# Kernel tuning notes

Measured on AMD Instinct MI355X. Metric: run time of the kernel, lower is better.

The kernel has to match this reference:

```python
import jax, jax.numpy as jnp
import numpy as np

B_SZ, L, D_MODEL = 2, 2048, 1024
EXPAND, D_STATE, D_CONV = 2, 16, 4
D_INNER = D_MODEL * EXPAND
DT_RANK = -(-D_MODEL // 16)  # ceil(d_model/16) = 64


def setup_inputs() -> dict:
    key = jax.random.key(0)
    ks = jax.random.split(key, 8)
    s = 0.02
    return {
        "u": jax.random.normal(ks[0], (B_SZ, L, D_MODEL), jnp.float32),
        "W_in": jax.random.normal(ks[1], (2 * D_INNER, D_MODEL), jnp.float32) * s,
        "W_out": jax.random.normal(ks[2], (D_MODEL, D_INNER), jnp.float32) * s,
        "conv_w": jax.random.normal(ks[3], (D_INNER, D_CONV), jnp.float32) * s,  # depthwise kernel (weight.squeeze(1))
        "conv_b": jax.random.normal(ks[4], (D_INNER,), jnp.float32) * s,
        "W_x": jax.random.normal(ks[5], (DT_RANK + 2 * D_STATE, D_INNER), jnp.float32) * s,
        "W_dt": jax.random.normal(ks[6], (D_INNER, DT_RANK), jnp.float32) * s,
        "b_dt": jax.random.normal(ks[7], (D_INNER,), jnp.float32) * s,
        "A_log": jnp.tile(jnp.log(jnp.arange(1, D_STATE + 1, dtype=jnp.float32)), (D_INNER, 1)),
        "D_param": jnp.ones((D_INNER,), jnp.float32),
    }


def _causal_conv(x, w, b):
    # x: [B, L, Di], w: [Di, K] depthwise, b: [Di]. Left-pad K-1 => causal.
    K = w.shape[1]
    Lx = x.shape[1]
    xp = jnp.pad(x, ((0, 0), (K - 1, 0), (0, 0)))
    acc = b
    for k in range(K):  # K=4, tiny fixed unroll
        acc = acc + xp[:, k:k + Lx, :] * w[:, k]
    return acc


def reference(u, W_in, W_out, conv_w, conv_b, W_x, W_dt, b_dt, A_log, D_param):
    d_inner = D_param.shape[0]
    N = A_log.shape[1]
    dt_rank = W_dt.shape[1]

    xz = u @ W_in.T                       # [B, L, 2*Di]
    x_in, z = xz[..., :d_inner], xz[..., d_inner:]
    x = jax.nn.silu(_causal_conv(x_in, conv_w, conv_b))  # [B, L, Di]

    x_p = x @ W_x.T                       # [B, L, dt_rank + 2N]
    dt_r = x_p[..., :dt_rank]
    Bm = x_p[..., dt_rank:dt_rank + N]    # [B, L, N]
    Cm = x_p[..., dt_rank + N:]           # [B, L, N]
    dt = jax.nn.softplus(dt_r @ W_dt.T + b_dt)  # [B, L, Di]

    A = -jnp.exp(A_log)                   # [Di, N]

    def step(h, inp):
        dt_t, B_t, C_t, x_t = inp         # [B,Di], [B,N], [B,N], [B,Di]
        dA = jnp.exp(dt_t[:, :, None] * A)             # [B, Di, N]
        h = dA * h + (dt_t * x_t)[:, :, None] * B_t[:, None, :]
        y_t = jnp.einsum('bdn,bn->bd', h, C_t)
        return h, y_t

    h0 = jnp.zeros((u.shape[0], d_inner, N), u.dtype)
    seq = (dt.transpose(1, 0, 2), Bm.transpose(1, 0, 2),
           Cm.transpose(1, 0, 2), x.transpose(1, 0, 2))
    _, ys = jax.lax.scan(step, h0, seq)   # ys: [L, B, Di]

    y = ys.transpose(1, 0, 2) + D_param * x
    y = y * jax.nn.silu(z)
    return y @ W_out.T                    # [B, L, d_model]
```

## Files before the change

kernel.cpp:

```cpp
#include <hip/hip_runtime.h>
#include <hip/hip_bf16.h>
#include <cstdint>
#include <cstddef>


typedef __bf16 bf16x8 __attribute__((ext_vector_type(8)));
typedef __bf16 bf16x4 __attribute__((ext_vector_type(4)));
typedef float f32x4 __attribute__((ext_vector_type(4)));
typedef unsigned int u32x4 __attribute__((ext_vector_type(4)));

#define LOG2E 1.44269504088896f

__device__ __forceinline__ bf16x8 cvt8(const float* __restrict__ p) {
    f32x4 a = *(const f32x4*)p;
    f32x4 b = *(const f32x4*)(p + 4);
    bf16x8 o;
    o[0] = (__bf16)a[0]; o[1] = (__bf16)a[1]; o[2] = (__bf16)a[2]; o[3] = (__bf16)a[3];
    o[4] = (__bf16)b[0]; o[5] = (__bf16)b[1]; o[6] = (__bf16)b[2]; o[7] = (__bf16)b[3];
    return o;
}

__device__ __forceinline__ void gll16(const __bf16* g, __bf16* l) {
    __builtin_amdgcn_global_load_lds(
        (const __attribute__((address_space(1))) void*)g,
        (__attribute__((address_space(3))) void*)l, 16, 0, 0);
}

__device__ __forceinline__ uint32_t packbf(__bf16 lo, __bf16 hi) {
    uint16_t a = __builtin_bit_cast(uint16_t, lo);
    uint16_t b = __builtin_bit_cast(uint16_t, hi);
    return (uint32_t)a | ((uint32_t)b << 16);
}
__device__ __forceinline__ float lo2f(uint32_t u) { return __builtin_bit_cast(float, u << 16); }
__device__ __forceinline__ float hi2f(uint32_t u) { return __builtin_bit_cast(float, u & 0xffff0000u); }

template<int CTRL>
__device__ __forceinline__ float qp_add(float v) {
    int r = __builtin_amdgcn_update_dpp(0, __builtin_bit_cast(int, v), CTRL, 0xF, 0xF, true);
    return v + __builtin_bit_cast(float, r);
}

__global__ void cvt_all_kernel(const float* __restrict__ u,   __bf16* __restrict__ ub,
                               const float* __restrict__ wi,  __bf16* __restrict__ wib,
                               const float* __restrict__ wo,  __bf16* __restrict__ wob,
                               const float* __restrict__ wx,  __bf16* __restrict__ wxb,
                               const float* __restrict__ wdt, __bf16* __restrict__ wdtb,
                               const float* __restrict__ cw,  float* __restrict__ cwT) {
    int i = blockIdx.x * 256 + threadIdx.x;
    if (i < 1351680) {
        const float* s; __bf16* d; int off;
        if (i < 524288)                { s = u;   d = ub;   off = i; }
        else if (i < 1048576)          { s = wi;  d = wib;  off = i - 524288; }
        else if (i < 1310720)          { s = wo;  d = wob;  off = i - 1048576; }
        else if (i < 1335296)          { s = wx;  d = wxb;  off = i - 1310720; }
        else                           { s = wdt; d = wdtb; off = i - 1335296; }
        *(bf16x8*)(d + (size_t)off * 8) = cvt8(s + (size_t)off * 8);
    } else {
        int off = (i - 1351680) * 8;
#pragma unroll
        for (int e = 0; e < 8; ++e) {
            int s = off + e;
            cwT[(s & 3) * 2048 + (s >> 2)] = cw[s];
        }
    }
}

__global__ __launch_bounds__(256, 3) void gemm_async_bf(const __bf16* __restrict__ A,
                                                        const __bf16* __restrict__ Bw,
                                                        __bf16* __restrict__ C,
                                                        int K, int ldc) {
    __shared__ __bf16 As[128][32];
    __shared__ __bf16 Bs[128][32];
    const int tid = threadIdx.x, lane = tid & 63, wave = tid >> 6;
    const int m0 = blockIdx.x * 128, n0 = blockIdx.y * 128;
    const int wm = (wave >> 1) * 64, wn = (wave & 1) * 64;
    const int mrow = lane & 15, kq = (lane >> 4) * 8;
    const int sr = wave * 32 + (lane >> 2);
    const int sk = (lane & 3) * 8;
    const __bf16* Ag0 = A + (size_t)(m0 + sr) * K + sk;
    const __bf16* Ag1 = Ag0 + (size_t)16 * K;
    const __bf16* Bg0 = Bw + (size_t)(n0 + sr) * K + sk;
    const __bf16* Bg1 = Bg0 + (size_t)16 * K;
    __bf16* La0 = &As[wave * 32][0];
    __bf16* La1 = &As[wave * 32 + 16][0];
    __bf16* Lb0 = &Bs[wave * 32][0];
    __bf16* Lb1 = &Bs[wave * 32 + 16][0];
    f32x4 acc[4][4] = {};
    for (int k0 = 0; k0 < K; k0 += 32) {
        gll16(Ag0 + k0, La0);
        gll16(Ag1 + k0, La1);
        gll16(Bg0 + k0, Lb0);
        gll16(Bg1 + k0, Lb1);
        __syncthreads();
        bf16x8 af[4], bfr[4];
#pragma unroll
        for (int i = 0; i < 4; ++i) af[i]  = *(const bf16x8*)&As[wm + i * 16 + mrow][kq];
#pragma unroll
        for (int j = 0; j < 4; ++j) bfr[j] = *(const bf16x8*)&Bs[wn + j * 16 + mrow][kq];
#pragma unroll
        for (int i = 0; i < 4; ++i)
#pragma unroll
            for (int j = 0; j < 4; ++j)
                acc[i][j] = __builtin_amdgcn_mfma_f32_16x16x32_bf16(af[i], bfr[j], acc[i][j], 0, 0, 0);
        __syncthreads();
    }
    const int col = lane & 15;
    const int rb = (lane >> 4) * 4;
#pragma unroll
    for (int i = 0; i < 4; ++i)
#pragma unroll
        for (int j = 0; j < 4; ++j)
#pragma unroll
            for (int r = 0; r < 4; ++r)
                C[(size_t)(m0 + wm + i * 16 + rb + r) * ldc + n0 + wn + j * 16 + col] =
                    (__bf16)acc[i][j][r];
}

__global__ __launch_bounds__(256, 3) void gemm_splitk(const __bf16* __restrict__ A,
                                                      const __bf16* __restrict__ Bw,
                                                      float* __restrict__ P) {
    __shared__ __bf16 As[128][32];
    __shared__ __bf16 Bs[128][32];
    const int tid = threadIdx.x, lane = tid & 63, wave = tid >> 6;
    const int m0 = blockIdx.x * 128, n0 = blockIdx.y * 128;
    const int kz = blockIdx.z * 1024;
    const int wm = (wave >> 1) * 64, wn = (wave & 1) * 64;
    const int mrow = lane & 15, kq = (lane >> 4) * 8;
    const int sr = wave * 32 + (lane >> 2);
    const int sk = (lane & 3) * 8;
    const __bf16* Ag0 = A + (size_t)(m0 + sr) * 2048 + kz + sk;
    const __bf16* Ag1 = Ag0 + (size_t)16 * 2048;
    const __bf16* Bg0 = Bw + (size_t)(n0 + sr) * 2048 + kz + sk;
    const __bf16* Bg1 = Bg0 + (size_t)16 * 2048;
    __bf16* La0 = &As[wave * 32][0];
    __bf16* La1 = &As[wave * 32 + 16][0];
    __bf16* Lb0 = &Bs[wave * 32][0];
    __bf16* Lb1 = &Bs[wave * 32 + 16][0];
    f32x4 acc[4][4] = {};
    for (int k0 = 0; k0 < 1024; k0 += 32) {
        gll16(Ag0 + k0, La0);
        gll16(Ag1 + k0, La1);
        gll16(Bg0 + k0, Lb0);
        gll16(Bg1 + k0, Lb1);
        __syncthreads();
        bf16x8 af[4], bfr[4];
#pragma unroll
        for (int i = 0; i < 4; ++i) af[i]  = *(const bf16x8*)&As[wm + i * 16 + mrow][kq];
#pragma unroll
        for (int j = 0; j < 4; ++j) bfr[j] = *(const bf16x8*)&Bs[wn + j * 16 + mrow][kq];
#pragma unroll
        for (int i = 0; i < 4; ++i)
#pragma unroll
            for (int j = 0; j < 4; ++j)
                acc[i][j] = __builtin_amdgcn_mfma_f32_16x16x32_bf16(af[i], bfr[j], acc[i][j], 0, 0, 0);
        __syncthreads();
    }
    const int col = lane & 15;
    const int rb = (lane >> 4) * 4;
    float* Pz = P + (size_t)blockIdx.z * 4096 * 1024;
#pragma unroll
    for (int i = 0; i < 4; ++i)
#pragma unroll
        for (int j = 0; j < 4; ++j)
#pragma unroll
            for (int r = 0; r < 4; ++r)
                Pz[(size_t)(m0 + wm + i * 16 + rb + r) * 1024 + n0 + wn + j * 16 + col] =
                    acc[i][j][r];
}

__global__ void add2_kernel(const float* __restrict__ P, float* __restrict__ out) {
    int i = blockIdx.x * 256 + threadIdx.x;
    f32x4 a = *(const f32x4*)(P + (size_t)i * 4);
    f32x4 b = *(const f32x4*)(P + (size_t)4096 * 1024 + (size_t)i * 4);
    *(f32x4*)(out + (size_t)i * 4) = a + b;
}

__global__ void conv_silu_kernel(const __bf16* __restrict__ xz,
                                 const float* __restrict__ cwT,
                                 const float* __restrict__ cb,
                                 __bf16* __restrict__ x) {
    int tid = threadIdx.x;
    int r = blockIdx.x;
    int l = r & 2047;
    int d = tid * 8;

    float acc[8];
    {
        f32x4 b0 = *(const f32x4*)(cb + d);
        f32x4 b1 = *(const f32x4*)(cb + d + 4);
#pragma unroll
        for (int i = 0; i < 4; ++i) { acc[i] = b0[i]; acc[4 + i] = b1[i]; }
    }

#pragma unroll
    for (int dlt = 0; dlt < 4; ++dlt) {
        if (l - dlt >= 0) {
            bf16x8 v = *(const bf16x8*)(xz + (size_t)(r - dlt) * 4096 + d);
            f32x4 w0 = *(const f32x4*)(cwT + (3 - dlt) * 2048 + d);
            f32x4 w1 = *(const f32x4*)(cwT + (3 - dlt) * 2048 + d + 4);
#pragma unroll
            for (int i = 0; i < 4; ++i) {
                acc[i]     = fmaf((float)v[i],     w0[i], acc[i]);
                acc[4 + i] = fmaf((float)v[4 + i], w1[i], acc[4 + i]);
            }
        }
    }
    bf16x8 o;
#pragma unroll
    for (int i = 0; i < 8; ++i) {
        float s = acc[i];
        s = s / (1.f + __expf(-s));
        o[i] = (__bf16)s;
    }
    *(bf16x8*)(x + (size_t)r * 2048 + d) = o;
}

__global__ __launch_bounds__(256, 2) void gemm_xp_split(const __bf16* __restrict__ A,
                                                        const __bf16* __restrict__ Bw,
                                                        float* __restrict__ P) {
    __shared__ __bf16 As[64][64];
    __shared__ __bf16 Bs[96][64];
    const int tid = threadIdx.x;
    const int lane = tid & 63;
    const int wave = tid >> 6;
    const int m0 = blockIdx.x * 64;
    const int kb = blockIdx.y * 256;
    const int mrow = lane & 15;
    const int kq = (lane >> 4) * 8;

    f32x4 acc[6] = {};

    for (int k0 = kb; k0 < kb + 256; k0 += 64) {
#pragma unroll
        for (int r = 0; r < 2; ++r) {
            int e = r * 256 + tid;
            int row = e >> 3, kc = e & 7;
            *(bf16x8*)&As[row][kc * 8] =
                *(const bf16x8*)(A + (size_t)(m0 + row) * 2048 + k0 + kc * 8);
        }
#pragma unroll
        for (int r = 0; r < 3; ++r) {
            int e = r * 256 + tid;
            int row = e >> 3, kc = e & 7;
            *(bf16x8*)&Bs[row][kc * 8] =
                *(const bf16x8*)(Bw + (size_t)row * 2048 + k0 + kc * 8);
        }
        __syncthreads();
#pragma unroll
        for (int kc = 0; kc < 2; ++kc) {
            bf16x8 af = *(const bf16x8*)&As[wave * 16 + mrow][kc * 32 + kq];
#pragma unroll
            for (int j = 0; j < 6; ++j) {
                bf16x8 bfr = *(const bf16x8*)&Bs[j * 16 + mrow][kc * 32 + kq];
                acc[j] = __builtin_amdgcn_mfma_f32_16x16x32_bf16(af, bfr, acc[j], 0, 0, 0);
            }
        }
        __syncthreads();
    }
    const int col = lane & 15;
    const int rb = (lane >> 4) * 4;
    float* Pb = P + (size_t)blockIdx.y * 4096 * 96;
#pragma unroll
    for (int j = 0; j < 6; ++j)
#pragma unroll
        for (int r = 0; r < 4; ++r)
            Pb[(size_t)(m0 + wave * 16 + rb + r) * 96 + j * 16 + col] = acc[j][r];
}

__global__ void xp_reduce(const float* __restrict__ P, __bf16* __restrict__ xp) {
    int m = blockIdx.x, c = threadIdx.x;
    if (c < 96) {
        float s = 0.f;
#pragma unroll
        for (int k = 0; k < 8; ++k) s += P[(size_t)k * 4096 * 96 + (size_t)m * 96 + c];
        xp[(size_t)m * 96 + c] = (__bf16)s;
    }
}

__global__ __launch_bounds__(256, 2) void gemm_dt(const __bf16* __restrict__ xp,
                                                  const __bf16* __restrict__ Wdt,
                                                  const float* __restrict__ bdt,
                                                  __bf16* __restrict__ dt) {
    const int tid = threadIdx.x;
    const int lane = tid & 63;
    const int wave = tid >> 6;
    const int m0 = blockIdx.x * 128 + (wave >> 1) * 64;
    const int n0 = blockIdx.y * 128 + (wave & 1) * 64;
    const int mrow = lane & 15;
    const int kq = (lane >> 4) * 8;

    f32x4 acc[4][4] = {};
#pragma unroll
    for (int kc = 0; kc < 2; ++kc) {
        bf16x8 af[4], bfr[4];
#pragma unroll
        for (int i = 0; i < 4; ++i)
            af[i] = *(const bf16x8*)(xp + (size_t)(m0 + i * 16 + mrow) * 96 + kc * 32 + kq);
#pragma unroll
        for (int j = 0; j < 4; ++j)
            bfr[j] = *(const bf16x8*)(Wdt + (size_t)(n0 + j * 16 + mrow) * 64 + kc * 32 + kq);
#pragma unroll
        for (int i = 0; i < 4; ++i)
#pragma unroll
            for (int j = 0; j < 4; ++j)
                acc[i][j] = __builtin_amdgcn_mfma_f32_16x16x32_bf16(af[i], bfr[j], acc[i][j], 0, 0, 0);
    }
    const int col = lane & 15;
    const int rb = (lane >> 4) * 4;
#pragma unroll
    for (int i = 0; i < 4; ++i)
#pragma unroll
        for (int j = 0; j < 4; ++j) {
            int cc = n0 + j * 16 + col;
            float bias = bdt[cc];
#pragma unroll
            for (int r = 0; r < 4; ++r) {
                float v = acc[i][j][r] + bias;
                float sp = (v > 20.f) ? v : log1pf(__expf(v));
                dt[(size_t)(m0 + i * 16 + rb + r) * 4096 + cc] = (__bf16)sp;
            }
        }
}

__global__ __launch_bounds__(256, 6) void scan_p1(const __bf16* __restrict__ xz,
                                                  const __bf16* __restrict__ xq,
                                                  const __bf16* __restrict__ xp,
                                                  const float* __restrict__ A_log,
                                                  float* __restrict__ h_end,
                                                  float* __restrict__ dtsum) {
    __shared__ uint32_t s_dtx[64][64];
    __shared__ __bf16 s_B[64][16];
    const int tid = threadIdx.x;
    const int bi = blockIdx.x;
    const int b = bi >> 10, c = (bi >> 5) & 31, d0 = (bi & 31) * 64;
    const int row0 = b * 2048 + c * 64;

    const int lane = tid & 63, wave = tid >> 6;
    const int dcol = wave * 16 + (lane >> 2);
    const int d = d0 + dcol;
    const int ng = lane & 3;
    f32x4 Al = *(const f32x4*)(A_log + (size_t)d * 16 + ng * 4);
    float Adn2[4];
#pragma unroll
    for (int j = 0; j < 4; ++j) Adn2[j] = -__expf(Al[j]) * LOG2E;

    {
        int t = tid >> 2, g = (tid & 3) * 4;
        *(bf16x4*)&s_B[t][g] = *(const bf16x4*)(xp + (size_t)(row0 + t) * 96 + 64 + g);
    }
#pragma unroll
    for (int i = 0; i < 4; ++i) {
        int w = i * 256 + tid;
        int t = w >> 4, g = (w & 15) * 4;
        size_t r = (size_t)(row0 + t);
        bf16x4 dt4 = *(const bf16x4*)(xz + r * 4096 + d0 + g);
        bf16x4 x4  = *(const bf16x4*)(xq + r * 2048 + d0 + g);
        u32x4 o;
#pragma unroll
        for (int k = 0; k < 4; ++k) o[k] = packbf(dt4[k], x4[k]);
        *(u32x4*)&s_dtx[t][g] = o;
    }
    __syncthreads();

    float h[4] = {0.f, 0.f, 0.f, 0.f};
    float ds = 0.f;
#pragma unroll 8
    for (int t = 0; t < 64; ++t) {
        uint32_t u = s_dtx[t][dcol];
        float dt = lo2f(u), x = hi2f(u);
        bf16x4 B4 = *(const bf16x4*)&s_B[t][ng * 4];
        float p = dt * x;
#pragma unroll
        for (int j = 0; j < 4; ++j) {
            float dA = exp2f(dt * Adn2[j]);
            h[j] = fmaf(dA, h[j], p * (float)B4[j]);
        }
        ds += dt;
    }
    size_t base = (size_t)(b * 32 + c) * 2048 + d;
    f32x4 hv = {h[0], h[1], h[2], h[3]};
    *(f32x4*)(h_end + base * 16 + ng * 4) = hv;
    if (ng == 0) dtsum[base] = ds;
}

__global__ __launch_bounds__(256) void scan_p2(const float* __restrict__ A_log,
                                               const float* __restrict__ dtsum,
                                               const float* __restrict__ h_end,
                                               float* __restrict__ h_in) {
    int idx = blockIdx.x * 256 + threadIdx.x;
    int b = idx >> 15, rem = idx & 32767;
    int d = rem >> 4;
    float Adn = -__expf(A_log[rem]);
    float h = 0.f;
#pragma unroll
    for (int c = 0; c < 32; ++c) {
        size_t base = ((size_t)(b * 32 + c) << 15) + rem;
        h_in[base] = h;
        float P = __expf(Adn * dtsum[((size_t)(b * 32 + c) << 11) + d]);
        h = fmaf(P, h, h_end[base]);
    }
}

__global__ __launch_bounds__(256, 4) void scan_p3(const __bf16* __restrict__ xz,
                                                  __bf16* __restrict__ xq,
                                                  const __bf16* __restrict__ xp,
                                                  const float* __restrict__ A_log,
                                                  const float* __restrict__ Dp,
                                                  const float* __restrict__ h_in) {
    __shared__ uint32_t s_dtx[64][64];
    __shared__ uint32_t s_BC[64][16];
    __shared__ __bf16 s_y[64][64];
    const int tid = threadIdx.x;
    const int bi = blockIdx.x;
    const int b = bi >> 10, c = (bi >> 5) & 31, d0 = (bi & 31) * 64;
    const int row0 = b * 2048 + c * 64;

    const int lane = tid & 63, wave = tid >> 6;
    const int dcol = wave * 16 + (lane >> 2);
    const int d = d0 + dcol;
    const int ng = lane & 3;
    f32x4 Al = *(const f32x4*)(A_log + (size_t)d * 16 + ng * 4);
    float Adn2[4];
#pragma unroll
    for (int j = 0; j < 4; ++j) Adn2[j] = -__expf(Al[j]) * LOG2E;
    const float Dd = Dp[d];
    f32x4 h = *(const f32x4*)(h_in + ((size_t)(b * 32 + c) * 2048 + d) * 16 + ng * 4);

    {
        int t = tid >> 2, g = (tid & 3) * 4;
        bf16x4 B4 = *(const bf16x4*)(xp + (size_t)(row0 + t) * 96 + 64 + g);
        bf16x4 C4 = *(const bf16x4*)(xp + (size_t)(row0 + t) * 96 + 80 + g);
        u32x4 o;
#pragma unroll
        for (int k = 0; k < 4; ++k) o[k] = packbf(B4[k], C4[k]);
        *(u32x4*)&s_BC[t][g] = o;
    }
#pragma unroll
    for (int i = 0; i < 4; ++i) {
        int w = i * 256 + tid;
        int t = w >> 4, g = (w & 15) * 4;
        size_t r = (size_t)(row0 + t);
        bf16x4 dt4 = *(const bf16x4*)(xz + r * 4096 + d0 + g);
        bf16x4 x4  = *(const bf16x4*)(xq + r * 2048 + d0 + g);
        u32x4 o;
#pragma unroll
        for (int k = 0; k < 4; ++k) o[k] = packbf(dt4[k], x4[k]);
        *(u32x4*)&s_dtx[t][g] = o;
    }
    __syncthreads();

#pragma unroll 8
    for (int t = 0; t < 64; ++t) {
        uint32_t u = s_dtx[t][dcol];
        float dt = lo2f(u), x = hi2f(u);
        u32x4 bc = *(const u32x4*)&s_BC[t][ng * 4];
        float p = dt * x;
        float cs;
#pragma unroll
        for (int j = 0; j < 4; ++j) {
            float Bv = lo2f(bc[j]), Cv = hi2f(bc[j]);
            float dA = exp2f(dt * Adn2[j]);
            h[j] = fmaf(dA, h[j], p * Bv);
            cs = (j == 0) ? h[0] * Cv : fmaf(h[j], Cv, cs);
        }
        cs = qp_add<0xB1>(cs);
        cs = qp_add<0x4E>(cs);
        if (ng == 0) s_y[t][dcol] = (__bf16)fmaf(Dd, x, cs);
    }
    __syncthreads();
#pragma unroll
    for (int i = 0; i < 2; ++i) {
        int w = i * 256 + tid;
        int t = w >> 3, g = (w & 7) * 8;
        bf16x8 z8 = *(const bf16x8*)(xz + (size_t)(row0 + t) * 4096 + 2048 + d0 + g);
        bf16x8 y8 = *(bf16x8*)&s_y[t][g];
        bf16x8 o;
#pragma unroll
        for (int k = 0; k < 8; ++k) {
            float zv = (float)z8[k];
            float yv = (float)y8[k] * (zv / (1.f + __expf(-zv)));
            o[k] = (__bf16)yv;
        }
        *(bf16x8*)(xq + (size_t)(row0 + t) * 2048 + d0 + g) = o;
    }
}

extern "C" void kernel_launch(void* const* d_in, const int* in_sizes, int n_in,
                              void* d_out, int out_size, void* d_ws, size_t ws_size,
                              hipStream_t stream) {
    const float* u      = (const float*)d_in[0];
    const float* W_in   = (const float*)d_in[1];
    const float* W_out  = (const float*)d_in[2];
    const float* conv_w = (const float*)d_in[3];
    const float* conv_b = (const float*)d_in[4];
    const float* W_x    = (const float*)d_in[5];
    const float* W_dt   = (const float*)d_in[6];
    const float* b_dt   = (const float*)d_in[7];
    const float* A_log  = (const float*)d_in[8];
    const float* D_p    = (const float*)d_in[9];
    float* out = (float*)d_out;

    __bf16* xz   = (__bf16*)d_ws;
    __bf16* xq   = xz  + (size_t)4096 * 4096;
    __bf16* xp   = xq  + (size_t)4096 * 2048;
    __bf16* Wib  = xp  + (size_t)4096 * 96;
    __bf16* Wob  = Wib + (size_t)4096 * 1024;
    __bf16* Wxb  = Wob + (size_t)1024 * 2048;
    __bf16* Wdtb = Wxb + (size_t)96 * 2048;

    __bf16* ub    = (__bf16*)d_out;
    float* xpart  = (float*)d_out;
    float* h_end  = (float*)d_out;
    float* h_in   = (float*)d_out + 2097152;
    float* cwT    = (float*)d_out + 3407872;
    float* dtsum  = (float*)Wib;
    float* gpart  = (float*)xz;

    cvt_all_kernel<<<5284, 256, 0, stream>>>(u, ub, W_in, Wib, W_out, Wob,
                                             W_x, Wxb, W_dt, Wdtb, conv_w, cwT);

    gemm_async_bf<<<dim3(32, 32), 256, 0, stream>>>(ub, Wib, xz, 1024, 4096);
    conv_silu_kernel<<<4096, 256, 0, stream>>>(xz, cwT, conv_b, xq);
    gemm_xp_split<<<dim3(64, 8), 256, 0, stream>>>(xq, Wxb, xpart);
    xp_reduce<<<4096, 128, 0, stream>>>(xpart, xp);
    gemm_dt<<<dim3(32, 16), 256, 0, stream>>>(xp, Wdtb, b_dt, xz);
    scan_p1<<<2048, 256, 0, stream>>>(xz, xq, xp, A_log, h_end, dtsum);
    scan_p2<<<256, 256, 0, stream>>>(A_log, dtsum, h_end, h_in);
    scan_p3<<<2048, 256, 0, stream>>>(xz, xq, xp, A_log, D_p, h_in);
    gemm_splitk<<<dim3(32, 8, 2), 256, 0, stream>>>(xq, Wob, gpart);
    add2_kernel<<<4096, 256, 0, stream>>>(gpart, out);
}
```

Baseline: 333.8 us.

## Fuse three-phase chunked scan into one cooperative kernel with grid syncs

Replaces the three scan kernels with a single cooperative kernel. Each block loads its 128-step chunk of dt, x, B and C into LDS once, runs the local scan, grid-syncs, does the inter-chunk carry on the first 256 blocks, grid-syncs again, then applies the correction and the z gating in place. This avoids reloading chunk data and the extra launches, at the cost of grid-wide barriers and an occupancy requirement of 4 blocks per CU, with a fallback path when that requirement is not met. The depthwise conv kernel also now handles 4 rows per block with a sliding window, so overlapping rows are reused instead of reloaded.

```diff
diff --git a/kernel.cpp b/kernel.cpp
--- a/kernel.cpp
+++ b/kernel.cpp
@@ -1,8 +1,11 @@
 #include <hip/hip_runtime.h>
 #include <hip/hip_bf16.h>
+#include <hip/hip_cooperative_groups.h>
 #include <cstdint>
 #include <cstddef>
 
+
+namespace cg = cooperative_groups;
 
 typedef __bf16 bf16x8 __attribute__((ext_vector_type(8)));
 typedef __bf16 bf16x4 __attribute__((ext_vector_type(4)));
@@ -33,6 +36,10 @@
 }
 __device__ __forceinline__ float lo2f(uint32_t u) { return __builtin_bit_cast(float, u << 16); }
 __device__ __forceinline__ float hi2f(uint32_t u) { return __builtin_bit_cast(float, u & 0xffff0000u); }
+__device__ __forceinline__ uint32_t f2hi(float y, uint32_t u) {
+    uint16_t yb = __builtin_bit_cast(uint16_t, (__bf16)y);
+    return (u & 0xffffu) | ((uint32_t)yb << 16);
+}
 
 template<int CTRL>
 __device__ __forceinline__ float qp_add(float v) {
@@ -179,40 +186,53 @@
                                  const float* __restrict__ cwT,
                                  const float* __restrict__ cb,
                                  __bf16* __restrict__ x) {
-    int tid = threadIdx.x;
-    int r = blockIdx.x;
-    int l = r & 2047;
-    int d = tid * 8;
-
-    float acc[8];
-    {
-        f32x4 b0 = *(const f32x4*)(cb + d);
-        f32x4 b1 = *(const f32x4*)(cb + d + 4);
+    const int r0 = blockIdx.x * 4;
+    const int d = threadIdx.x * 8;
+    const bool first = (r0 & 2047) == 0;
+
+    f32x4 w0[4], w1[4];
+#pragma unroll
+    for (int k = 0; k < 4; ++k) {
+        w0[k] = *(const f32x4*)(cwT + k * 2048 + d);
+        w1[k] = *(const f32x4*)(cwT + k * 2048 + d + 4);
+    }
+    f32x4 b0 = *(const f32x4*)(cb + d);
+    f32x4 b1 = *(const f32x4*)(cb + d + 4);
+
+    bf16x8 win[4];
+#pragma unroll
+    for (int i = 0; i < 3; ++i) {
+        if (first) {
+#pragma unroll
+            for (int k = 0; k < 8; ++k) win[i][k] = (__bf16)0.f;
+        } else {
+            win[i] = *(const bf16x8*)(xz + (size_t)(r0 - 3 + i) * 4096 + d);
+        }
+    }
+#pragma unroll
+    for (int rr = 0; rr < 4; ++rr) {
+        win[(rr + 3) & 3] = *(const bf16x8*)(xz + (size_t)(r0 + rr) * 4096 + d);
+        float acc[8];
 #pragma unroll
         for (int i = 0; i < 4; ++i) { acc[i] = b0[i]; acc[4 + i] = b1[i]; }
-    }
-
-#pragma unroll
-    for (int dlt = 0; dlt < 4; ++dlt) {
-        if (l - dlt >= 0) {
-            bf16x8 v = *(const bf16x8*)(xz + (size_t)(r - dlt) * 4096 + d);
-            f32x4 w0 = *(const f32x4*)(cwT + (3 - dlt) * 2048 + d);
-            f32x4 w1 = *(const f32x4*)(cwT + (3 - dlt) * 2048 + d + 4);
+#pragma unroll
+        for (int k = 0; k < 4; ++k) {
+            bf16x8 v = win[(rr + k) & 3];
 #pragma unroll
             for (int i = 0; i < 4; ++i) {
-                acc[i]     = fmaf((float)v[i],     w0[i], acc[i]);
-                acc[4 + i] = fmaf((float)v[4 + i], w1[i], acc[4 + i]);
+                acc[i]     = fmaf((float)v[i],     w0[k][i], acc[i]);
+                acc[4 + i] = fmaf((float)v[4 + i], w1[k][i], acc[4 + i]);
             }
         }
-    }
-    bf16x8 o;
-#pragma unroll
-    for (int i = 0; i < 8; ++i) {
-        float s = acc[i];
-        s = s / (1.f + __expf(-s));
-        o[i] = (__bf16)s;
-    }
-    *(bf16x8*)(x + (size_t)r * 2048 + d) = o;
+        bf16x8 o;
+#pragma unroll
+        for (int i = 0; i < 8; ++i) {
+            float s = acc[i];
+            s = s / (1.f + __expf(-s));
+            o[i] = (__bf16)s;
+        }
+        *(bf16x8*)(x + (size_t)(r0 + rr) * 2048 + d) = o;
+    }
 }
 
 __global__ __launch_bounds__(256, 2) void gemm_xp_split(const __bf16* __restrict__ A,
@@ -320,6 +340,146 @@
                 dt[(size_t)(m0 + i * 16 + rb + r) * 4096 + cc] = (__bf16)sp;
             }
         }
+}
+
+__global__ __launch_bounds__(256, 4) void scan_fused(const __bf16* __restrict__ xz,
+                                                     __bf16* __restrict__ xq,
+                                                     const __bf16* __restrict__ xp,
+                                                     const float* __restrict__ A_log,
+                                                     const float* __restrict__ Dp,
+                                                     float* __restrict__ h_end,
+                                                     float* __restrict__ dtsum,
+                                                     float* __restrict__ h_in) {
+    __shared__ uint32_t s_dtx[128][64];
+    __shared__ uint32_t s_BC[128][16];
+    const int tid = threadIdx.x;
+    const int bi = blockIdx.x;
+    const int b = bi >> 9, c = (bi >> 5) & 15, d0 = (bi & 31) * 64;
+    const int row0 = b * 2048 + c * 128;
+
+    const int lane = tid & 63, wave = tid >> 6;
+    const int dcol = wave * 16 + (lane >> 2);
+    const int d = d0 + dcol;
+    const int ng = lane & 3;
+    f32x4 Al = *(const f32x4*)(A_log + (size_t)d * 16 + ng * 4);
+    float Adn2[4];
+#pragma unroll
+    for (int j = 0; j < 4; ++j) Adn2[j] = -__expf(Al[j]) * LOG2E;
+    const float Dd = Dp[d];
+
+#pragma unroll
+    for (int i = 0; i < 8; ++i) {
+        int w = i * 256 + tid;
+        int t = w >> 4, g = (w & 15) * 4;
+        size_t r = (size_t)(row0 + t);
+        bf16x4 dt4 = *(const bf16x4*)(xz + r * 4096 + d0 + g);
+        bf16x4 x4  = *(const bf16x4*)(xq + r * 2048 + d0 + g);
+        u32x4 o;
+#pragma unroll
+        for (int k = 0; k < 4; ++k) o[k] = packbf(dt4[k], x4[k]);
+        *(u32x4*)&s_dtx[t][g] = o;
+    }
+#pragma unroll
+    for (int i = 0; i < 2; ++i) {
+        int w = i * 256 + tid;
+        int t = w >> 2, g = (w & 3) * 4;
+        bf16x4 B4 = *(const bf16x4*)(xp + (size_t)(row0 + t) * 96 + 64 + g);
+        bf16x4 C4 = *(const bf16x4*)(xp + (size_t)(row0 + t) * 96 + 80 + g);
+        u32x4 o;
+#pragma unroll
+        for (int k = 0; k < 4; ++k) o[k] = packbf(B4[k], C4[k]);
+        *(u32x4*)&s_BC[t][g] = o;
+    }
+    __syncthreads();
+
+    {
+        float h[4] = {0.f, 0.f, 0.f, 0.f};
+        float ds = 0.f;
+#pragma unroll 4
+        for (int t = 0; t < 128; ++t) {
+            uint32_t u = s_dtx[t][dcol];
+            float dt = lo2f(u), x = hi2f(u);
+            u32x4 bc = *(const u32x4*)&s_BC[t][ng * 4];
+            float p = dt * x;
+            float cs;
+#pragma unroll
+            for (int j = 0; j < 4; ++j) {
+                float Bv = lo2f(bc[j]), Cv = hi2f(bc[j]);
+                float dA = exp2f(dt * Adn2[j]);
+                h[j] = fmaf(dA, h[j], p * Bv);
+                cs = (j == 0) ? h[0] * Cv : fmaf(h[j], Cv, cs);
+            }
+            ds += dt;
+            cs = qp_add<0xB1>(cs);
+            cs = qp_add<0x4E>(cs);
+            if (ng == 0) s_dtx[t][dcol] = f2hi(fmaf(Dd, x, cs), u);
+        }
+        size_t base = (size_t)(b * 16 + c) * 2048 + d;
+        f32x4 hv = {h[0], h[1], h[2], h[3]};
+        *(f32x4*)(h_end + base * 16 + ng * 4) = hv;
+        if (ng == 0) dtsum[base] = ds;
+    }
+
+    cg::this_grid().sync();
+
+    if (bi < 256) {
+        int idx = bi * 256 + tid;
+        int bb = idx >> 15, rem = idx & 32767;
+        int dd = rem >> 4;
+        float Adn = -__expf(A_log[rem]);
+        float h = 0.f;
+#pragma unroll
+        for (int cc = 0; cc < 16; ++cc) {
+            size_t base = ((size_t)(bb * 16 + cc) << 15) + rem;
+            h_in[base] = h;
+            float P = __expf(Adn * dtsum[((size_t)(bb * 16 + cc) << 11) + dd]);
+            h = fmaf(P, h, h_end[base]);
+        }
+    }
+
+    cg::this_grid().sync();
+
+    {
+        f32x4 hin = *(const f32x4*)(h_in + ((size_t)(b * 16 + c) * 2048 + d) * 16 + ng * 4);
+        float Sd = 0.f;
+#pragma unroll 4
+        for (int t = 0; t < 128; ++t) {
+            uint32_t u = s_dtx[t][dcol];
+            float dt = lo2f(u);
+            Sd += dt;
+            u32x4 bc = *(const u32x4*)&s_BC[t][ng * 4];
+            float corr;
+#pragma unroll
+            for (int j = 0; j < 4; ++j) {
+                float Cv = hi2f(bc[j]);
+                float e = exp2f(Sd * Adn2[j]);
+                corr = (j == 0) ? e * hin[0] * Cv : fmaf(e * hin[j], Cv, corr);
+            }
+            corr = qp_add<0xB1>(corr);
+            corr = qp_add<0x4E>(corr);
+            if (ng == 0) {
+                float yraw = hi2f(u) + corr;
+                s_dtx[t][dcol] = __builtin_bit_cast(uint32_t, yraw);
+            }
+        }
+    }
+    __syncthreads();
+
+#pragma unroll
+    for (int i = 0; i < 8; ++i) {
+        int w = i * 256 + tid;
+        int t = w >> 4, g = (w & 15) * 4;
+        u32x4 yv = *(const u32x4*)&s_dtx[t][g];
+        bf16x4 z4 = *(const bf16x4*)(xz + (size_t)(row0 + t) * 4096 + 2048 + d0 + g);
+        bf16x4 o;
+#pragma unroll
+        for (int k = 0; k < 4; ++k) {
+            float zv = (float)z4[k];
+            float yv_f = __builtin_bit_cast(float, yv[k]);
+            o[k] = (__bf16)(yv_f * (zv / (1.f + __expf(-zv))));
+        }
+        *(bf16x4*)(xq + (size_t)(row0 + t) * 2048 + d0 + g) = o;
+    }
 }
 
 __global__ __launch_bounds__(256, 6) void scan_p1(const __bf16* __restrict__ xz,
@@ -520,13 +680,30 @@
                                              W_x, Wxb, W_dt, Wdtb, conv_w, cwT);
 
     gemm_async_bf<<<dim3(32, 32), 256, 0, stream>>>(ub, Wib, xz, 1024, 4096);
-    conv_silu_kernel<<<4096, 256, 0, stream>>>(xz, cwT, conv_b, xq);
+    conv_silu_kernel<<<1024, 256, 0, stream>>>(xz, cwT, conv_b, xq);
     gemm_xp_split<<<dim3(64, 8), 256, 0, stream>>>(xq, Wxb, xpart);
     xp_reduce<<<4096, 128, 0, stream>>>(xpart, xp);
     gemm_dt<<<dim3(32, 16), 256, 0, stream>>>(xp, Wdtb, b_dt, xz);
-    scan_p1<<<2048, 256, 0, stream>>>(xz, xq, xp, A_log, h_end, dtsum);
-    scan_p2<<<256, 256, 0, stream>>>(A_log, dtsum, h_end, h_in);
-    scan_p3<<<2048, 256, 0, stream>>>(xz, xq, xp, A_log, D_p, h_in);
+
+    int maxb = 0;
+    hipError_t qerr = hipOccupancyMaxActiveBlocksPerMultiprocessor(&maxb, scan_fused, 256, 0);
+    bool coop_ok = (qerr == hipSuccess) && (maxb >= 4);
+    if (coop_ok) {
+        const __bf16* xz_c = xz; __bf16* xq_c = xq; const __bf16* xp_c = xp;
+        const float* al_c = A_log; const float* dp_c = D_p;
+        float* he_c = h_end; float* ds_c = dtsum; float* hi_c = h_in;
+        void* args[] = {&xz_c, &xq_c, &xp_c, &al_c, &dp_c, &he_c, &ds_c, &hi_c};
+        hipError_t lerr = hipLaunchCooperativeKernel((const void*)scan_fused,
+                                                     dim3(1024), dim3(256),
+                                                     args, 0, stream);
+        if (lerr != hipSuccess) coop_ok = false;
+    }
+    if (!coop_ok) {
+        scan_p1<<<2048, 256, 0, stream>>>(xz, xq, xp, A_log, h_end, dtsum);
+        scan_p2<<<256, 256, 0, stream>>>(A_log, dtsum, h_end, h_in);
+        scan_p3<<<2048, 256, 0, stream>>>(xz, xq, xp, A_log, D_p, h_in);
+    }
+
     gemm_splitk<<<dim3(32, 8, 2), 256, 0, stream>>>(xq, Wob, gpart);
     add2_kernel<<<4096, 256, 0, stream>>>(gpart, out);
 }
```

Measured after the change: 335.6 us. About the same (+0.5%).
